# Kernel optimization log

Hardware: AMD Instinct MI355X
Metric: run time of the kernel (lower is better)

## Reference

```python
import jax, jax.numpy as jnp
import numpy as np

DIM = 1024
H = 16
D = DIM // H
SCALE = D ** -0.5
EPS = 1e-5


def _layernorm(x, w, b):
    # force_fp32 LayerNorm over last axis
    xf = x.astype(jnp.float32)
    mu = xf.mean(-1, keepdims=True)
    var = xf.var(-1, keepdims=True)
    y = (xf - mu) / jnp.sqrt(var + EPS) * w.astype(jnp.float32) + b.astype(jnp.float32)
    return y.astype(x.dtype)


def setup_inputs() -> dict:
    key = jax.random.key(0)
    ks = jax.random.split(key, 8)
    x = jax.random.normal(ks[0], (2, 2048, DIM), dtype=jnp.float32)
    qkv_w = jax.random.normal(ks[1], (3 * DIM, DIM), dtype=jnp.float32) * (DIM ** -0.5)
    q_norm_w = jnp.ones((D,), jnp.float32)
    q_norm_b = jnp.zeros((D,), jnp.float32)
    k_norm_w = jnp.ones((D,), jnp.float32)
    k_norm_b = jnp.zeros((D,), jnp.float32)
    proj_w = jax.random.normal(ks[2], (DIM, DIM), dtype=jnp.float32) * (DIM ** -0.5)
    proj_b = jnp.zeros((DIM,), jnp.float32)
    return {"x": x, "qkv_w": qkv_w, "q_norm_w": q_norm_w, "q_norm_b": q_norm_b,
            "k_norm_w": k_norm_w, "k_norm_b": k_norm_b, "proj_w": proj_w, "proj_b": proj_b}


def reference(x, qkv_w, q_norm_w, q_norm_b, k_norm_w, k_norm_b, proj_w, proj_b):
    B, N, C = x.shape
    qkv = x @ qkv_w.T                                  # [B,N,3C]
    qkv = qkv.reshape(B, N, 3, H, D).transpose(2, 0, 3, 1, 4)  # [3,B,H,N,D]
    q, k, v = qkv[0], qkv[1], qkv[2]
    # per-head QK LayerNorm over head_dim
    q = _layernorm(q, q_norm_w, q_norm_b)
    k = _layernorm(k, k_norm_w, k_norm_b)
    # k-centering across sequence
    k = k - k.mean(-2, keepdims=True)
    attn = jnp.einsum('bhnd,bhmd->bhnm', q * SCALE, k)
    attn = attn - attn.max(-1, keepdims=True)
    attn = jax.nn.softmax(attn, axis=-1)
    out = jnp.einsum('bhnm,bhmd->bhnd', attn, v)       # [B,H,N,D]
    out = out.transpose(0, 2, 1, 3).reshape(B, N, C)
    return out @ proj_w.T + proj_b
```

## Files before the change

### kernel.cpp

```cpp
#include <hip/hip_runtime.h>
#include <cstdint>
#include <cstddef>

#define SEQ     2048
#define NBATCH  2
#define CDIM    1024
#define NHEAD   16
#define HDIM    64
#define MTOT    (NBATCH*SEQ)
#define C3      (3*CDIM)
#define LOG2E   1.44269504088896340736f
#define QKSCALE (0.125f*LOG2E)
#define LN_EPS  1e-5f

typedef unsigned short u16;
typedef short s16x8 __attribute__((ext_vector_type(8)));
typedef float f32x4  __attribute__((ext_vector_type(4)));
typedef float f32x16 __attribute__((ext_vector_type(16)));

static __device__ __forceinline__ f32x4 mfma16(s16x8 a, s16x8 b, f32x4 c) {
  return __builtin_amdgcn_mfma_f32_16x16x32_bf16(a, b, c, 0, 0, 0);
}
static __device__ __forceinline__ f32x16 mfma32(s16x8 a, s16x8 b, f32x16 c) {
  return __builtin_amdgcn_mfma_f32_32x32x16_bf16(a, b, c, 0, 0, 0);
}
static __device__ __forceinline__ float b2f(u16 v) {
  return __uint_as_float(((unsigned)v) << 16);
}
static __device__ __forceinline__ u16 f2b(float f) {
  unsigned u = __float_as_uint(f);
  u = u + 0x7fffu + ((u >> 16) & 1u);
  return (u16)(u >> 16);
}
static __device__ __forceinline__ float fexp2(float x) {
  float r;
  asm("v_exp_f32 %0, %1" : "=v"(r) : "v"(x));
  return r;
}

#define G2L16(g, l) __builtin_amdgcn_global_load_lds( \
    (__attribute__((address_space(1))) void*)(g),     \
    (__attribute__((address_space(3))) void*)(l), 16, 0, 0)

#define XSEG   (MTOT*CDIM/8)
#define W1SEG  (C3*CDIM/8)
#define W2SEG  (CDIM*CDIM/8)
__global__ __launch_bounds__(256) void cast_all(
    const float* __restrict__ x, const float* __restrict__ w1,
    const float* __restrict__ w2, u16* __restrict__ xb,
    u16* __restrict__ wqkv, u16* __restrict__ wproj)
{
  int i = blockIdx.x * 256 + threadIdx.x;
  const float* src; u16* dst; int off;
  if (i < XSEG)              { src = x;  dst = xb;    off = i; }
  else if (i < XSEG + W1SEG) { src = w1; dst = wqkv;  off = i - XSEG; }
  else                       { src = w2; dst = wproj; off = i - XSEG - W1SEG; }
  float4 a = ((const float4*)src)[2*off];
  float4 b = ((const float4*)src)[2*off+1];
  union { u16 u[8]; uint4 v; } r;
  r.u[0]=f2b(a.x); r.u[1]=f2b(a.y); r.u[2]=f2b(a.z); r.u[3]=f2b(a.w);
  r.u[4]=f2b(b.x); r.u[5]=f2b(b.y); r.u[6]=f2b(b.z); r.u[7]=f2b(b.w);
  ((uint4*)dst)[off] = r.v;
}

template<bool WRITE_BF16, bool BIAS>
__global__ __launch_bounds__(256) void gemm_nt(
    const u16* __restrict__ A, const u16* __restrict__ Bm,
    void* __restrict__ Cout, const float* __restrict__ bias,
    int M, int Nn, int K)
{
  __shared__ u16 As[128*64];
  __shared__ u16 Bs[128*64];
  const int tid = threadIdx.x;
  const int wave = tid >> 6, lane = tid & 63;
  const int l15 = lane & 15, l4 = lane >> 4;
  const int m0 = blockIdx.x * 128, n0 = blockIdx.y * 128;
  const int wr = (wave >> 1) * 64, wc = (wave & 1) * 64;
  f32x4 acc[4][4] = {};

  for (int k0 = 0; k0 < K; k0 += 64) {
    if (k0) __syncthreads();
#pragma unroll
    for (int i = 0; i < 4; ++i) {
      int ci  = (i*4 + wave)*64 + lane;
      int row = ci >> 3, ch = ci & 7;
      int chs = ch ^ (row & 7);
      const u16* ga = A  + (size_t)(m0 + row)*K + k0 + chs*8;
      const u16* gb = Bm + (size_t)(n0 + row)*K + k0 + chs*8;
      G2L16(ga, As + (i*4 + wave)*512);
      G2L16(gb, Bs + (i*4 + wave)*512);
    }
    __syncthreads();

#pragma unroll
    for (int kk = 0; kk < 2; ++kk) {
      s16x8 af[4], bf[4];
#pragma unroll
      for (int r = 0; r < 4; ++r) {
        int row = wr + r*16 + l15;
        af[r] = *(const s16x8*)(As + row*64 + (((kk*4 + l4) ^ (row & 7))*8));
      }
#pragma unroll
      for (int c = 0; c < 4; ++c) {
        int row = wc + c*16 + l15;
        bf[c] = *(const s16x8*)(Bs + row*64 + (((kk*4 + l4) ^ (row & 7))*8));
      }
#pragma unroll
      for (int r = 0; r < 4; ++r)
#pragma unroll
        for (int c = 0; c < 4; ++c)
          acc[r][c] = mfma16(af[r], bf[c], acc[r][c]);
    }
  }

#pragma unroll
  for (int r = 0; r < 4; ++r)
#pragma unroll
    for (int c = 0; c < 4; ++c) {
      int row = m0 + wr + r*16 + l4*4;
      int col = n0 + wc + c*16 + l15;
#pragma unroll
      for (int q = 0; q < 4; ++q) {
        float v = acc[r][c][q];
        if (BIAS) v += bias[col];
        if (WRITE_BF16) ((u16*)Cout)[(size_t)(row + q)*Nn + col] = f2b(v);
        else           ((float*)Cout)[(size_t)(row + q)*Nn + col] = v;
      }
    }
}

__global__ __launch_bounds__(256) void ln_qk(
    const u16* __restrict__ qkv,
    const float* __restrict__ qw, const float* __restrict__ qb,
    const float* __restrict__ kw, const float* __restrict__ kb,
    u16* __restrict__ Qs, u16* __restrict__ Kn)
{
  int gw   = blockIdx.x * 4 + (threadIdx.x >> 6);
  int lane = threadIdx.x & 63;
  int m = gw >> 4, h = gw & 15;
  const u16* rowp = qkv + (size_t)m*C3 + h*HDIM + lane;
  int b = m >> 11, n = m & 2047;
  size_t o = ((size_t)(b*NHEAD + h)*SEQ + n)*HDIM + lane;

  float wq = qw[lane], bq = qb[lane], wk = kw[lane], bk = kb[lane];
  float xq = b2f(rowp[0]);
  float xk = b2f(rowp[CDIM]);
  float sq = xq, s2q = xq*xq, sk = xk, s2k = xk*xk;
#pragma unroll
  for (int off = 32; off; off >>= 1) {
    sq += __shfl_xor(sq, off, 64);  s2q += __shfl_xor(s2q, off, 64);
    sk += __shfl_xor(sk, off, 64);  s2k += __shfl_xor(s2k, off, 64);
  }
  float muq = sq*(1.f/64.f), varq = s2q*(1.f/64.f) - muq*muq;
  float muk = sk*(1.f/64.f), vark = s2k*(1.f/64.f) - muk*muk;
  float yq = (xq - muq) * (1.f/sqrtf(varq + LN_EPS)) * wq + bq;
  float yk = (xk - muk) * (1.f/sqrtf(vark + LN_EPS)) * wk + bk;
  Qs[o] = f2b(yq * QKSCALE);
  Kn[o] = f2b(yk);
}

__global__ __launch_bounds__(256) void v_transpose(
    const u16* __restrict__ qkv, u16* __restrict__ Vt)
{
  __shared__ u16 t[64][80];
  int bh = blockIdx.x, j0 = blockIdx.y * 64;
  int b = bh >> 4, h = bh & 15;
  int tid = threadIdx.x;
  int nl = tid >> 2, ch = tid & 3;
  const u16* src = qkv + (size_t)(b*SEQ + j0 + nl)*C3 + 2*CDIM + h*HDIM + ch*16;
  *(uint4*)&t[nl][ch*16]     = *(const uint4*)src;
  *(uint4*)&t[nl][ch*16 + 8] = *(const uint4*)(src + 8);
  __syncthreads();
  int d = tid >> 2, nc = tid & 3;
  u16 o[16];
#pragma unroll
  for (int i = 0; i < 16; ++i) o[i] = t[nc*16 + i][d];
  u16* dst = Vt + ((size_t)(bh*HDIM + d))*SEQ + j0 + nc*16;
  *(uint4*)dst       = *(uint4*)&o[0];
  *(uint4*)(dst + 8) = *(uint4*)&o[8];
}

__global__ __launch_bounds__(256) void flash_attn(
    const u16* __restrict__ Qs, const u16* __restrict__ Kn,
    const u16* __restrict__ Vt, u16* __restrict__ Oa)
{
  __shared__ u16 Kt[3][64*64];
  const int tid = threadIdx.x, wave = tid >> 6, lane = tid & 63;
  const int l31 = lane & 31, hi = lane >> 5;
  const int bid0 = blockIdx.x + blockIdx.y*16;
  const int nid  = (bid0 & 7)*64 + (bid0 >> 3);
  const int bh   = nid >> 4;
  const int q0   = (nid & 15)*128 + wave*32;
  const int sw = l31 & 7;

  const u16* Qrow = Qs + ((size_t)bh*SEQ + q0 + l31)*HDIM + hi*8;
  s16x8 qf[4];
#pragma unroll
  for (int ks = 0; ks < 4; ++ks)
    qf[ks] = *(const s16x8*)(Qrow + ks*16);

  f32x16 o0 = {}, o1 = {};
  float l_run = 0.f;

  const u16* Kg = Kn + (size_t)bh*SEQ*HDIM;
  const u16* Vg = Vt + (size_t)bh*HDIM*SEQ;

  auto STAGEK = [&](int jb, int buf) {
#pragma unroll
    for (int i = 0; i < 2; ++i) {
      int ci = (i*4 + wave)*64 + lane;
      int row = ci >> 3, ch = ci & 7;
      int chs = ch ^ (row & 7);
      G2L16(Kg + (size_t)(jb + row)*HDIM + chs*8, Kt[buf] + (i*4 + wave)*512);
    }
  };
  auto LOADV = [&](int jb, s16x8* vf) {
#pragma unroll
    for (int s = 0; s < 4; ++s) {
      vf[s]   = *(const s16x8*)(Vg + (size_t)l31*SEQ      + jb + (s*2+hi)*8);
      vf[4+s] = *(const s16x8*)(Vg + (size_t)(32+l31)*SEQ + jb + (s*2+hi)*8);
    }
  };

  auto TILE = [&](const u16* Kb, const s16x8* vf) {
    f32x16 s0 = {}, s1 = {};
    __builtin_amdgcn_s_setprio(1);
#pragma unroll
    for (int ks = 0; ks < 4; ++ks) {
      int ch = ((ks*2 + hi) ^ sw) * 8;
      s16x8 k0 = *(const s16x8*)(Kb + l31*64 + ch);
      s16x8 k1 = *(const s16x8*)(Kb + (32 + l31)*64 + ch);
      s0 = mfma32(k0, qf[ks], s0);
      s1 = mfma32(k1, qf[ks], s1);
    }
    __builtin_amdgcn_s_setprio(0);

    float p0[16], p1[16];
#pragma unroll
    for (int i = 0; i < 16; ++i) p0[i] = fexp2(s0[i]);
#pragma unroll
    for (int i = 0; i < 16; ++i) p1[i] = fexp2(s1[i]);
    float s8[8];
#pragma unroll
    for (int i = 0; i < 8; ++i) s8[i] = (p0[i] + p0[i+8]) + (p1[i] + p1[i+8]);
    l_run += ((s8[0]+s8[1]) + (s8[2]+s8[3])) + ((s8[4]+s8[5]) + (s8[6]+s8[7]));

    s16x8 pf[4];
#pragma unroll
    for (int f = 0; f < 2; ++f) {
      const float* pp = f ? p1 : p0;
      unsigned pk[4][2];
#pragma unroll
      for (int q = 0; q < 4; ++q)
#pragma unroll
        for (int i = 0; i < 2; ++i)
          asm("v_cvt_pk_bf16_f32 %0, %1, %2"
              : "=v"(pk[q][i]) : "v"(pp[4*q+2*i]), "v"(pp[4*q+2*i+1]));
#pragma unroll
      for (int kc = 0; kc < 2; ++kc) {
        union { unsigned u[4]; s16x8 v; } bfu;
#pragma unroll
        for (int i = 0; i < 2; ++i) {
          unsigned x = pk[2*kc][i], y = pk[2*kc+1][i];
          asm("v_permlane32_swap_b32 %0, %1" : "+v"(x), "+v"(y));
          bfu.u[i] = x; bfu.u[2+i] = y;
        }
        pf[2*f+kc] = bfu.v;
      }
    }

    __builtin_amdgcn_s_setprio(1);
#pragma unroll
    for (int s = 0; s < 4; ++s) {
      o0 = mfma32(vf[s],   pf[s], o0);
      o1 = mfma32(vf[4+s], pf[s], o1);
    }
    __builtin_amdgcn_s_setprio(0);
  };

  s16x8 vA[8], vB[8];
  STAGEK(0, 0);
  STAGEK(64, 1);
  LOADV(0, vA);
  asm volatile("s_waitcnt vmcnt(8)" ::: "memory");

  const int NT = SEQ/64;
  for (int t = 0; t < NT; t += 2) {
    __builtin_amdgcn_s_barrier();
    __builtin_amdgcn_sched_barrier(0);
    if (t + 2 < NT) STAGEK((t+2)*64, (t+2)%3);
    LOADV((t+1)*64, vB);
    TILE(Kt[t%3], vA);
    __builtin_amdgcn_s_barrier();
    __builtin_amdgcn_sched_barrier(0);
    if (t + 3 < NT) STAGEK((t+3)*64, (t+3)%3);
    if (t + 2 < NT) LOADV((t+2)*64, vA);
    TILE(Kt[(t+1)%3], vB);
  }

  float l_all = l_run + __shfl_xor(l_run, 32, 64);
  float inv = 1.f / l_all;
  int b = bh >> 4, h = bh & 15;
  u16* dst = Oa + ((size_t)(b*SEQ + q0 + l31))*CDIM + h*HDIM;
#pragma unroll
  for (int df = 0; df < 2; ++df)
#pragma unroll
    for (int q2 = 0; q2 < 4; ++q2) {
      float a0, a1, a2, a3;
      if (df) { a0=o1[4*q2]; a1=o1[4*q2+1]; a2=o1[4*q2+2]; a3=o1[4*q2+3]; }
      else    { a0=o0[4*q2]; a1=o0[4*q2+1]; a2=o0[4*q2+2]; a3=o0[4*q2+3]; }
      a0 *= inv; a1 *= inv; a2 *= inv; a3 *= inv;
      unsigned w0, w1;
      asm("v_cvt_pk_bf16_f32 %0, %1, %2" : "=v"(w0) : "v"(a0), "v"(a1));
      asm("v_cvt_pk_bf16_f32 %0, %1, %2" : "=v"(w1) : "v"(a2), "v"(a3));
      uint2 st; st.x = w0; st.y = w1;
      *(uint2*)(dst + df*32 + q2*8 + hi*4) = st;
    }
}

extern "C" void kernel_launch(void* const* d_in, const int* in_sizes, int n_in,
                              void* d_out, int out_size, void* d_ws, size_t ws_size,
                              hipStream_t stream)
{
  const float* x      = (const float*)d_in[0];
  const float* qkv_w  = (const float*)d_in[1];
  const float* qnw    = (const float*)d_in[2];
  const float* qnb    = (const float*)d_in[3];
  const float* knw    = (const float*)d_in[4];
  const float* knb    = (const float*)d_in[5];
  const float* proj_w = (const float*)d_in[6];
  const float* proj_b = (const float*)d_in[7];
  float* out = (float*)d_out;

  char* ws = (char*)d_ws;
  u16* xb    = (u16*)(ws);
  u16* wqkv  = (u16*)(ws + (8ull  << 20));
  u16* wproj = (u16*)(ws + (14ull << 20));
  u16* qkvb  = (u16*)(ws + (16ull << 20));
  u16* Qsb   = (u16*)(ws + (40ull << 20));
  u16* Knb   = (u16*)(ws + (48ull << 20));
  u16* Vtb   = (u16*)(ws + (56ull << 20));
  u16* Oab   = (u16*)(ws + (64ull << 20));

  cast_all<<<(XSEG + W1SEG + W2SEG)/256, 256, 0, stream>>>(
      x, qkv_w, proj_w, xb, wqkv, wproj);

  gemm_nt<true, false><<<dim3(MTOT/128, C3/128), 256, 0, stream>>>(
      xb, wqkv, qkvb, nullptr, MTOT, C3, CDIM);

  ln_qk<<<(MTOT*NHEAD)/4, 256, 0, stream>>>(qkvb, qnw, qnb, knw, knb, Qsb, Knb);
  v_transpose<<<dim3(NBATCH*NHEAD, SEQ/64), 256, 0, stream>>>(qkvb, Vtb);

  flash_attn<<<dim3(SEQ/128, NBATCH*NHEAD), 256, 0, stream>>>(Qsb, Knb, Vtb, Oab);

  gemm_nt<false, true><<<dim3(MTOT/128, CDIM/128), 256, 0, stream>>>(
      Oab, wproj, out, proj_b, MTOT, CDIM, CDIM);
}
```

Measured before the change: 232.2 us.

## Stage V through LDS with double buffering and shrink attention blocks to two waves

The flash attention kernel now stages both K and V tiles into shared memory with async global-to-LDS copies. It uses a simple two-buffer ping-pong with one __syncthreads per 64-key tile, replacing the triple-buffered K plus register-prefetched V pipeline. Blocks shrink from 4 waves (128 queries) to 2 waves (64 queries), the grid doubles, and the XCD-aware block-ID remapping is dropped. This trades register pressure and direct V global loads for more LDS traffic, lower K/V reuse per block and more frequent full barriers.

Result: faster. 217.4 us (-6.4%).

```diff
diff --git a/kernel.cpp b/kernel.cpp
--- a/kernel.cpp
+++ b/kernel.cpp
@@ -180,17 +180,15 @@
   *(uint4*)(dst + 8) = *(uint4*)&o[8];
 }
 
-__global__ __launch_bounds__(256) void flash_attn(
+__global__ __launch_bounds__(128) void flash_attn(
     const u16* __restrict__ Qs, const u16* __restrict__ Kn,
     const u16* __restrict__ Vt, u16* __restrict__ Oa)
 {
-  __shared__ u16 Kt[3][64*64];
+  __shared__ u16 Kt[2][64*64];
+  __shared__ u16 Vs[2][64*64];
   const int tid = threadIdx.x, wave = tid >> 6, lane = tid & 63;
   const int l31 = lane & 31, hi = lane >> 5;
-  const int bid0 = blockIdx.x + blockIdx.y*16;
-  const int nid  = (bid0 & 7)*64 + (bid0 >> 3);
-  const int bh   = nid >> 4;
-  const int q0   = (nid & 15)*128 + wave*32;
+  const int bh = blockIdx.y, q0 = blockIdx.x*64 + wave*32;
   const int sw = l31 & 7;
 
   const u16* Qrow = Qs + ((size_t)bh*SEQ + q0 + l31)*HDIM + hi*8;
@@ -205,24 +203,27 @@
   const u16* Kg = Kn + (size_t)bh*SEQ*HDIM;
   const u16* Vg = Vt + (size_t)bh*HDIM*SEQ;
 
-  auto STAGEK = [&](int jb, int buf) {
-#pragma unroll
-    for (int i = 0; i < 2; ++i) {
-      int ci = (i*4 + wave)*64 + lane;
+  auto STAGE = [&](int jb, int buf) {
+#pragma unroll
+    for (int i = 0; i < 4; ++i) {
+      int ci = (i*2 + wave)*64 + lane;
       int row = ci >> 3, ch = ci & 7;
       int chs = ch ^ (row & 7);
-      G2L16(Kg + (size_t)(jb + row)*HDIM + chs*8, Kt[buf] + (i*4 + wave)*512);
+      G2L16(Kg + (size_t)(jb + row)*HDIM + chs*8, Kt[buf] + (i*2 + wave)*512);
+      G2L16(Vg + (size_t)row*SEQ + jb + chs*8,    Vs[buf] + (i*2 + wave)*512);
     }
   };
-  auto LOADV = [&](int jb, s16x8* vf) {
-#pragma unroll
-    for (int s = 0; s < 4; ++s) {
-      vf[s]   = *(const s16x8*)(Vg + (size_t)l31*SEQ      + jb + (s*2+hi)*8);
-      vf[4+s] = *(const s16x8*)(Vg + (size_t)(32+l31)*SEQ + jb + (s*2+hi)*8);
-    }
-  };
-
-  auto TILE = [&](const u16* Kb, const s16x8* vf) {
+
+  STAGE(0, 0);
+  __syncthreads();
+
+  const int NT = SEQ/64;
+  for (int t = 0; t < NT; ++t) {
+    const int buf = t & 1;
+    if (t + 1 < NT) STAGE((t+1)*64, buf ^ 1);
+    const u16* Kb = Kt[buf];
+    const u16* Vb = Vs[buf];
+
     f32x16 s0 = {}, s1 = {};
     __builtin_amdgcn_s_setprio(1);
 #pragma unroll
@@ -272,30 +273,14 @@
     __builtin_amdgcn_s_setprio(1);
 #pragma unroll
     for (int s = 0; s < 4; ++s) {
-      o0 = mfma32(vf[s],   pf[s], o0);
-      o1 = mfma32(vf[4+s], pf[s], o1);
+      int ch = ((s*2 + hi) ^ sw) * 8;
+      s16x8 v0 = *(const s16x8*)(Vb + l31*64 + ch);
+      s16x8 v1 = *(const s16x8*)(Vb + (32 + l31)*64 + ch);
+      o0 = mfma32(v0, pf[s], o0);
+      o1 = mfma32(v1, pf[s], o1);
     }
     __builtin_amdgcn_s_setprio(0);
-  };
-
-  s16x8 vA[8], vB[8];
-  STAGEK(0, 0);
-  STAGEK(64, 1);
-  LOADV(0, vA);
-  asm volatile("s_waitcnt vmcnt(8)" ::: "memory");
-
-  const int NT = SEQ/64;
-  for (int t = 0; t < NT; t += 2) {
-    __builtin_amdgcn_s_barrier();
-    __builtin_amdgcn_sched_barrier(0);
-    if (t + 2 < NT) STAGEK((t+2)*64, (t+2)%3);
-    LOADV((t+1)*64, vB);
-    TILE(Kt[t%3], vA);
-    __builtin_amdgcn_s_barrier();
-    __builtin_amdgcn_sched_barrier(0);
-    if (t + 3 < NT) STAGEK((t+3)*64, (t+3)%3);
-    if (t + 2 < NT) LOADV((t+2)*64, vA);
-    TILE(Kt[(t+1)%3], vB);
+    __syncthreads();
   }
 
   float l_all = l_run + __shfl_xor(l_run, 32, 64);
@@ -351,7 +336,7 @@
   ln_qk<<<(MTOT*NHEAD)/4, 256, 0, stream>>>(qkvb, qnw, qnb, knw, knb, Qsb, Knb);
   v_transpose<<<dim3(NBATCH*NHEAD, SEQ/64), 256, 0, stream>>>(qkvb, Vtb);
 
-  flash_attn<<<dim3(SEQ/128, NBATCH*NHEAD), 256, 0, stream>>>(Qsb, Knb, Vtb, Oab);
+  flash_attn<<<dim3(SEQ/64, NBATCH*NHEAD), 128, 0, stream>>>(Qsb, Knb, Vtb, Oab);
 
   gemm_nt<false, true><<<dim3(MTOT/128, CDIM/128), 256, 0, stream>>>(
       Oab, wproj, out, proj_b, MTOT, CDIM, CDIM);
```
